# Performance work log

Hardware: AMD Instinct MI355X
Metric: run time of the kernel (lower is better)

## Reference

```python
import jax, jax.numpy as jnp
import numpy as np

B, R, C, D = 4, 64, 64, 512   # batch, rows, cols, hidden_size
H, DH = 4, 128                # num_heads, channels per head
S = R * C                     # flattened attention length (raster order)
NEG = -1e6                    # mask value used by coltran


def setup_inputs():
    key = jax.random.key(0)
    ks = jax.random.split(key, 7)
    def w(k, shape, s=0.02):
        return jax.random.normal(k, shape, jnp.float32) * s
    return dict(
        x=jax.random.normal(ks[0], (B, R, C, D), jnp.float32),
        wq=w(ks[1], (D, H, DH)),
        wk=w(ks[2], (D, H, DH)),
        wv=w(ks[3], (D, H, DH)),
        wo=w(ks[4], (H, DH, D)),
        # relative_attention_bias_i: [num_heads, 2*length] per axis
        # (zero-init in the original; randomized here so the bias path is exercised)
        rel_row=w(ks[5], (H, 2 * R)),
        rel_col=w(ks[6], (H, 2 * C)),
    )


def _axis_bias(w, L):
    """att_utils.relative_attn_bias: [H, 2L] -> [H, Lq, Lk], b[h,q,k] = w[h, L-1 + k - q]."""
    pos = jnp.arange(L)
    idx = (L - 1) + pos[None, :] - pos[:, None]  # [Lq, Lk] in [0, 2L-2]
    return w[:, idx]


def reference(x, wq, wk, wv, wo, rel_row, rel_col):
    # q/k/v projections: contract channel axis into [H, DH]
    q = jnp.einsum('brcd,dhe->brche', x, wq) * (DH ** -0.5)
    k = jnp.einsum('brcd,dhe->brche', x, wk)
    v = jnp.einsum('brcd,dhe->brche', x, wv)
    q = q.reshape(B, S, H, DH)
    k = k.reshape(B, S, H, DH)
    v = v.reshape(B, S, H, DH)

    # factorized N-D relative attention bias -> [H, S, S]
    brow = _axis_bias(rel_row, R)  # [H, R, R]
    bcol = _axis_bias(rel_col, C)  # [H, C, C]
    bias = (brow[:, :, None, :, None] + bcol[:, None, :, None, :]).reshape(H, S, S)

    # 'future' mask in raster order: disallow k > q
    mask = jnp.triu(jnp.full((S, S), NEG, dtype=jnp.float32), 1)

    logits = jnp.einsum('bqhe,bkhe->bhqk', q, k) + bias[None] + mask[None, None]
    p = jax.nn.softmax(logits, axis=-1)
    o = jnp.einsum('bhqk,bkhe->bqhe', p, v)       # weighted sum over keys
    out = jnp.einsum('bqhe,hed->bqd', o, wo)      # final projection, contract_axes=2
    return out.reshape(B, R, C, D)
```

## Files before the change

kernel.cpp:

```cpp
#include <hip/hip_runtime.h>
#include <cstdint>

typedef unsigned short u16;
typedef __attribute__((ext_vector_type(8))) short short8;
typedef __attribute__((ext_vector_type(4))) float f32x4;
typedef __attribute__((ext_vector_type(4))) unsigned short u16x4;
typedef __attribute__((ext_vector_type(2))) float f32x2;
typedef __attribute__((ext_vector_type(2))) __bf16 bf16x2;


__device__ __forceinline__ uint32_t pk2(float a, float b) {
  f32x2 t;
  t[0] = a;
  t[1] = b;
  bf16x2 h = __builtin_convertvector(t, bf16x2);
  return __builtin_bit_cast(uint32_t, h);
}

__device__ __forceinline__ u16 f2b(float f) {
  return __builtin_bit_cast(u16, (__bf16)f);
}

__device__ __forceinline__ uint2 pkbf16x4(f32x4 v, float s) {
  uint2 r;
  r.x = pk2(v[0] * s, v[1] * s);
  r.y = pk2(v[2] * s, v[3] * s);
  return r;
}

#define LDS_FENCE() asm volatile("s_waitcnt lgkmcnt(0)" ::: "memory")

__global__ __launch_bounds__(256) void xcast(const float* __restrict__ x,
                                             u16* __restrict__ xb) {
  const size_t i = (size_t)(blockIdx.x * 256 + threadIdx.x) * 8;
  const float4 a = *(const float4*)(x + i);
  const float4 b = *(const float4*)(x + i + 4);
  uint4 o;
  o.x = pk2(a.x, a.y);
  o.y = pk2(a.z, a.w);
  o.z = pk2(b.x, b.y);
  o.w = pk2(b.z, b.w);
  *(uint4*)(xb + i) = o;
}

__global__ __launch_bounds__(256) void transpose_all(const float* __restrict__ wq,
                                                     const float* __restrict__ wk,
                                                     const float* __restrict__ wv,
                                                     const float* __restrict__ wo,
                                                     u16* __restrict__ wT,
                                                     u16* __restrict__ woT) {
  __shared__ __align__(16) u16 T[64][68];
  const int mtx = blockIdx.y;
  const float* src = (mtx == 0) ? wq : (mtx == 1) ? wk : (mtx == 2) ? wv : wo;
  u16* dst = (mtx < 3) ? (wT + (size_t)mtx * 262144) : woT;
  const int tr = blockIdx.x >> 3, tc = blockIdx.x & 7;
  const int tid = threadIdx.x;
#pragma unroll
  for (int p = 0; p < 4; ++p) {
    int i = p * 256 + tid;
    int row = i >> 4, c4 = i & 15;
    float4 v = *(const float4*)(src + (size_t)(tr * 64 + row) * 512 + tc * 64 + c4 * 4);
    T[c4 * 4 + 0][row] = f2b(v.x);
    T[c4 * 4 + 1][row] = f2b(v.y);
    T[c4 * 4 + 2][row] = f2b(v.z);
    T[c4 * 4 + 3][row] = f2b(v.w);
  }
  __syncthreads();
#pragma unroll
  for (int p = 0; p < 4; ++p) {
    int i = p * 256 + tid;
    int row = i >> 4, c4 = i & 15;
    *(u16x4*)(dst + (size_t)(tc * 64 + row) * 512 + tr * 64 + c4 * 4) =
        *(const u16x4*)&T[row][c4 * 4];
  }
}

__global__ __launch_bounds__(512, 2) void qkv_gemm(const u16* __restrict__ xb,
                                                   const u16* __restrict__ wT_all,
                                                   u16* __restrict__ qbuf,
                                                   u16* __restrict__ kbuf,
                                                   u16* __restrict__ vtbuf) {
  __shared__ __align__(16) u16 smem[128 * 72 + 256 * 72];
  u16* As = smem;
  u16* Bs = smem + 128 * 72;
  const int tid = threadIdx.x;
  const int wave = tid >> 6, lane = tid & 63, quad = lane >> 4, l16 = lane & 15;
  const int wm = wave >> 2, wn = wave & 3;
  const int m0 = blockIdx.x * 128;
  const int which = blockIdx.y >> 1;
  const int n0 = (blockIdx.y & 1) * 256;
  const u16* wTb = wT_all + (size_t)which * 262144 + (size_t)n0 * 512;

  f32x4 acc[4][4];
  const f32x4 fz = {0.f, 0.f, 0.f, 0.f};
#pragma unroll
  for (int i = 0; i < 4; ++i)
#pragma unroll
    for (int j = 0; j < 4; ++j) acc[i][j] = fz;

  for (int k0 = 0; k0 < 512; k0 += 64) {
#pragma unroll
    for (int p = 0; p < 2; ++p) {
      int i = p * 512 + tid, row = i >> 3, c8 = i & 7;
      uint4 v = *(const uint4*)(xb + (size_t)(m0 + row) * 512 + k0 + c8 * 8);
      *(uint4*)&As[row * 72 + c8 * 8] = v;
    }
#pragma unroll
    for (int p = 0; p < 4; ++p) {
      int i = p * 512 + tid, row = i >> 3, c8 = i & 7;
      uint4 v = *(const uint4*)(wTb + (size_t)row * 512 + k0 + c8 * 8);
      *(uint4*)&Bs[row * 72 + c8 * 8] = v;
    }
    __syncthreads();
#pragma unroll
    for (int ks = 0; ks < 2; ++ks) {
      short8 xf[4], wf[4];
#pragma unroll
      for (int mt = 0; mt < 4; ++mt)
        xf[mt] = *(const short8*)&As[(wm * 64 + mt * 16 + l16) * 72 + ks * 32 + quad * 8];
#pragma unroll
      for (int nt = 0; nt < 4; ++nt)
        wf[nt] = *(const short8*)&Bs[(wn * 64 + nt * 16 + l16) * 72 + ks * 32 + quad * 8];
      if (which < 2) {
#pragma unroll
        for (int mt = 0; mt < 4; ++mt)
#pragma unroll
          for (int nt = 0; nt < 4; ++nt)
            acc[mt][nt] = __builtin_amdgcn_mfma_f32_16x16x32_bf16(wf[nt], xf[mt],
                                                                  acc[mt][nt], 0, 0, 0);
      } else {
#pragma unroll
        for (int mt = 0; mt < 4; ++mt)
#pragma unroll
          for (int nt = 0; nt < 4; ++nt)
            acc[mt][nt] = __builtin_amdgcn_mfma_f32_16x16x32_bf16(xf[mt], wf[nt],
                                                                  acc[mt][nt], 0, 0, 0);
      }
    }
    __syncthreads();
  }
  u16* sw = smem + wave * 3072;
  const int dhg0 = n0 + wn * 64;
  const int h = dhg0 >> 7, dhh0 = dhg0 & 127;
  const int bq = m0 >> 12;
  const int bh = bq * 4 + h;
  const int sl0 = (m0 & 4095) + wm * 64;

  if (which < 2) {
    const float scl = (which == 0) ? 0.08838834764831845f : 1.0f;
    u16* dst = (which == 0) ? qbuf : kbuf;
#pragma unroll
    for (int mt = 0; mt < 4; ++mt) {
      LDS_FENCE();
#pragma unroll
      for (int nt = 0; nt < 4; ++nt)
        *(uint2*)&sw[l16 * 68 + nt * 16 + quad * 4] = pkbf16x4(acc[mt][nt], scl);
      LDS_FENCE();
#pragma unroll
      for (int p = 0; p < 2; ++p) {
        const int sr = p * 8 + (lane >> 3), dl = (lane & 7) * 8;
        uint4 v = *(const uint4*)&sw[sr * 68 + dl];
        const int sl = sl0 + mt * 16 + sr;
        *(uint4*)(dst + ((size_t)(bh * 4096 + sl)) * 128 + dhh0 + dl) = v;
      }
    }
  } else {
#pragma unroll
    for (int p2 = 0; p2 < 2; ++p2) {
      LDS_FENCE();
#pragma unroll
      for (int m2 = 0; m2 < 2; ++m2) {
        const int mt = p2 * 2 + m2;
#pragma unroll
        for (int nt = 0; nt < 4; ++nt)
          *(uint2*)&sw[(nt * 16 + l16) * 36 + m2 * 16 + quad * 4] =
              pkbf16x4(acc[mt][nt], 1.0f);
      }
      LDS_FENCE();
#pragma unroll
      for (int j = 0; j < 4; ++j) {
        const int dl = j * 16 + (lane >> 2), so = (lane & 3) * 8;
        uint4 v = *(const uint4*)&sw[dl * 36 + so];
        const int sl = sl0 + p2 * 32 + so;
        *(uint4*)(vtbuf + ((size_t)(bh * 128 + dhh0 + dl)) * 4096 + sl) = v;
      }
    }
  }
}

__global__ __launch_bounds__(512, 4) void attn(const u16* __restrict__ qbuf,
                                               const u16* __restrict__ kbuf,
                                               const u16* __restrict__ vtbuf,
                                               const float* __restrict__ rel_row,
                                               const float* __restrict__ rel_col,
                                               u16* __restrict__ obuf) {
  __shared__ __align__(16) u16 Ks[64][136];
  __shared__ __align__(16) u16 Vt[128][72];
  __shared__ __align__(16) u16 Plds[8][16][72];
  __shared__ float rcol[128];
  __shared__ float rrow[128];

  const int tid = threadIdx.x;
  const int wave = tid >> 6, lane = tid & 63, quad = lane >> 4, l16 = lane & 15;
  const int bh = blockIdx.x & 15;
  const int qt = (blockIdx.x < 256) ? (31 - (blockIdx.x >> 4))
                                    : ((blockIdx.x >> 4) - 16);
  const int b = bh >> 2, h = bh & 3;

  if (tid < 128) rcol[tid] = rel_col[h * 128 + tid];
  else if (tid < 256) rrow[tid - 128] = rel_row[h * 128 + (tid - 128)];

  const int q_loc = wave * 16 + l16;
  const int q_glob = qt * 128 + q_loc;
  const int qr = 2 * qt + (wave >> 2);
  const int qc = q_glob & 63;

  const u16* qrow = qbuf + ((size_t)bh * 4096 + q_glob) * 128;
  short8 qf[4];
#pragma unroll
  for (int ks = 0; ks < 4; ++ks) qf[ks] = *(const short8*)(qrow + ks * 32 + quad * 8);

  __syncthreads();

  const float LOG2E = 1.4426950408889634f;
  float rc2[4][4];
#pragma unroll
  for (int nt = 0; nt < 4; ++nt)
#pragma unroll
    for (int r = 0; r < 4; ++r)
      rc2[nt][r] = rcol[63 + nt * 16 + quad * 4 + r - qc] * LOG2E;

  const f32x4 fz = {0.f, 0.f, 0.f, 0.f};
  f32x4 oacc[8];
#pragma unroll
  for (int i = 0; i < 8; ++i) oacc[i] = fz;
  float l_run = 0.0f;

  const u16* kbase = kbuf + (size_t)bh * 4096 * 128;
  const u16* vbase = vtbuf + (size_t)bh * 128 * 4096;
  const int kr = tid >> 4, kc = (tid & 15) * 8;
  const int vr = tid >> 3, vc = (tid & 7) * 8;

  uint4 kreg0, kreg1, vreg0, vreg1;
  {
    const u16* ksrc = kbase;
    const u16* vsrc = vbase;
    kreg0 = *(const uint4*)(ksrc + kr * 128 + kc);
    kreg1 = *(const uint4*)(ksrc + (32 + kr) * 128 + kc);
    vreg0 = *(const uint4*)(vsrc + (size_t)vr * 4096 + vc);
    vreg1 = *(const uint4*)(vsrc + (size_t)(64 + vr) * 4096 + vc);
  }

  const int ktmax = 2 * qt + 1;
  for (int kt = 0; kt <= ktmax; ++kt) {
    __syncthreads();
    *(uint4*)&Ks[kr][kc] = kreg0;
    *(uint4*)&Ks[32 + kr][kc] = kreg1;
    *(uint4*)&Vt[vr][vc] = vreg0;
    *(uint4*)&Vt[64 + vr][vc] = vreg1;
    __syncthreads();
    if (kt < ktmax) {
      const u16* ksrc = kbase + (kt + 1) * 64 * 128;
      const u16* vsrc = vbase + (kt + 1) * 64;
      kreg0 = *(const uint4*)(ksrc + kr * 128 + kc);
      kreg1 = *(const uint4*)(ksrc + (32 + kr) * 128 + kc);
      vreg0 = *(const uint4*)(vsrc + (size_t)vr * 4096 + vc);
      vreg1 = *(const uint4*)(vsrc + (size_t)(64 + vr) * 4096 + vc);
    }

    if (kt <= qr) {
      f32x4 sacc[4];
#pragma unroll
      for (int nt = 0; nt < 4; ++nt) sacc[nt] = fz;
#pragma unroll
      for (int ks = 0; ks < 4; ++ks)
#pragma unroll
        for (int nt = 0; nt < 4; ++nt) {
          short8 kf = *(const short8*)&Ks[nt * 16 + l16][ks * 32 + quad * 8];
          sacc[nt] = __builtin_amdgcn_mfma_f32_16x16x32_bf16(kf, qf[ks], sacc[nt], 0, 0, 0);
        }

      const float browl = rrow[63 + kt - qr] * LOG2E;
      const bool diag = (kt == qr);
#pragma unroll
      for (int nt = 0; nt < 4; ++nt) {
        f32x4 pv;
#pragma unroll
        for (int r = 0; r < 4; ++r) {
          const int kc2 = nt * 16 + quad * 4 + r;
          float p = __builtin_amdgcn_exp2f(fmaf(sacc[nt][r], LOG2E, rc2[nt][r] + browl));
          if (diag && kc2 > qc) p = 0.0f;
          l_run += p;
          pv[r] = p;
        }
        *(uint2*)&Plds[wave][l16][nt * 16 + quad * 4] = pkbf16x4(pv, 1.0f);
      }

#pragma unroll
      for (int ks2 = 0; ks2 < 2; ++ks2) {
        short8 pf = *(const short8*)&Plds[wave][l16][ks2 * 32 + quad * 8];
#pragma unroll
        for (int mt = 0; mt < 8; ++mt) {
          short8 vf = *(const short8*)&Vt[mt * 16 + l16][ks2 * 32 + quad * 8];
          oacc[mt] = __builtin_amdgcn_mfma_f32_16x16x32_bf16(vf, pf, oacc[mt], 0, 0, 0);
        }
      }
    }
  }

  l_run += __shfl_xor(l_run, 16);
  l_run += __shfl_xor(l_run, 32);
  const float inv_l = 1.0f / l_run;
  u16* orow = obuf + ((size_t)b * 4096 + q_glob) * 512 + h * 128;
#pragma unroll
  for (int mt = 0; mt < 8; ++mt)
    *(uint2*)(orow + mt * 16 + quad * 4) = pkbf16x4(oacc[mt], inv_l);
}

__global__ __launch_bounds__(512, 2) void out_gemm(const u16* __restrict__ obuf,
                                                   const u16* __restrict__ woT,
                                                   float* __restrict__ out) {
  __shared__ __align__(16) u16 smem[128 * 72 + 256 * 72];
  u16* As = smem;
  u16* Bs = smem + 128 * 72;
  const int tid = threadIdx.x;
  const int wave = tid >> 6, lane = tid & 63, quad = lane >> 4, l16 = lane & 15;
  const int wm = wave >> 2, wn = wave & 3;
  const int m0 = blockIdx.x * 128;
  const int n0 = blockIdx.y * 256;

  f32x4 acc[4][4];
  const f32x4 fz = {0.f, 0.f, 0.f, 0.f};
#pragma unroll
  for (int i = 0; i < 4; ++i)
#pragma unroll
    for (int j = 0; j < 4; ++j) acc[i][j] = fz;

  for (int k0 = 0; k0 < 512; k0 += 64) {
#pragma unroll
    for (int p = 0; p < 2; ++p) {
      int i = p * 512 + tid, row = i >> 3, c8 = i & 7;
      uint4 v = *(const uint4*)(obuf + (size_t)(m0 + row) * 512 + k0 + c8 * 8);
      *(uint4*)&As[row * 72 + c8 * 8] = v;
    }
#pragma unroll
    for (int p = 0; p < 4; ++p) {
      int i = p * 512 + tid, row = i >> 3, c8 = i & 7;
      uint4 v = *(const uint4*)(woT + (size_t)(n0 + row) * 512 + k0 + c8 * 8);
      *(uint4*)&Bs[row * 72 + c8 * 8] = v;
    }
    __syncthreads();
#pragma unroll
    for (int ks = 0; ks < 2; ++ks) {
      short8 of[4], wf[4];
#pragma unroll
      for (int mt = 0; mt < 4; ++mt)
        of[mt] = *(const short8*)&As[(wm * 64 + mt * 16 + l16) * 72 + ks * 32 + quad * 8];
#pragma unroll
      for (int nt = 0; nt < 4; ++nt)
        wf[nt] = *(const short8*)&Bs[(wn * 64 + nt * 16 + l16) * 72 + ks * 32 + quad * 8];
#pragma unroll
      for (int mt = 0; mt < 4; ++mt)
#pragma unroll
        for (int nt = 0; nt < 4; ++nt)
          acc[mt][nt] = __builtin_amdgcn_mfma_f32_16x16x32_bf16(wf[nt], of[mt],
                                                                acc[mt][nt], 0, 0, 0);
    }
    __syncthreads();
  }

  float* swf = (float*)smem + wave * 1536;
#pragma unroll
  for (int mt = 0; mt < 4; ++mt) {
    LDS_FENCE();
#pragma unroll
    for (int nt = 0; nt < 4; ++nt)
      *(f32x4*)&swf[l16 * 68 + nt * 16 + quad * 4] = acc[mt][nt];
    LDS_FENCE();
#pragma unroll
    for (int p = 0; p < 4; ++p) {
      const int sr = p * 4 + (lane >> 4), dl = l16 * 4;
      float4 v = *(const float4*)&swf[sr * 68 + dl];
      const int s = m0 + wm * 64 + mt * 16 + sr;
      *(float4*)(out + (size_t)s * 512 + n0 + wn * 64 + dl) = v;
    }
  }
}

extern "C" void kernel_launch(void* const* d_in, const int* in_sizes, int n_in,
                              void* d_out, int out_size, void* d_ws, size_t ws_size,
                              hipStream_t stream) {
  const float* x       = (const float*)d_in[0];
  const float* wq      = (const float*)d_in[1];
  const float* wk      = (const float*)d_in[2];
  const float* wv      = (const float*)d_in[3];
  const float* wo      = (const float*)d_in[4];
  const float* rel_row = (const float*)d_in[5];
  const float* rel_col = (const float*)d_in[6];
  float* out = (float*)d_out;

  char* ws = (char*)d_ws;
  u16* wT    = (u16*)(ws);
  u16* woT   = (u16*)(ws + 1572864);
  u16* qbuf  = (u16*)(ws + 2097152);
  u16* kbuf  = (u16*)(ws + 2097152 + 16777216);
  u16* vtbuf = (u16*)(ws + 2097152 + 2 * 16777216);
  u16* obuf  = (u16*)(ws + 2097152 + 3 * 16777216);
  u16* xb    = obuf;

  xcast<<<4096, 256, 0, stream>>>(x, xb);
  transpose_all<<<dim3(64, 4), 256, 0, stream>>>(wq, wk, wv, wo, wT, woT);
  qkv_gemm<<<dim3(128, 6), 512, 0, stream>>>(xb, wT, qbuf, kbuf, vtbuf);
  attn<<<512, 512, 0, stream>>>(qbuf, kbuf, vtbuf, rel_row, rel_col, obuf);
  out_gemm<<<dim3(128, 2), 512, 0, stream>>>(obuf, woT, out);
}
```

Before: 284.7 us.

## Restructure attention: 64-query blocks, direct global-to-LDS loads, swizzled LDS, register P

The attention kernel now uses 256-thread blocks covering 64 queries each (one image row), launched as 1024 blocks with a four-way load-balanced query-tile ordering. K and V tiles are fetched straight into XOR-swizzled LDS with global_load_lds instead of being staged through registers, and the LOG2E scale is folded into the bias tables. When the 16x16x16 MFMA builtin is available, P stays in registers and feeds the PV MFMA directly, skipping the LDS round trip. Wave priority hints are set around the MFMA loops. In exchange, the next tile is no longer prefetched, so the loads are exposed between the two barriers of each iteration, and K/V tiles are reloaded by twice as many blocks.

```diff
diff --git a/kernel.cpp b/kernel.cpp
--- a/kernel.cpp
+++ b/kernel.cpp
@@ -3,11 +3,18 @@
 
 typedef unsigned short u16;
 typedef __attribute__((ext_vector_type(8))) short short8;
+typedef __attribute__((ext_vector_type(4))) short short4v;
 typedef __attribute__((ext_vector_type(4))) float f32x4;
 typedef __attribute__((ext_vector_type(4))) unsigned short u16x4;
 typedef __attribute__((ext_vector_type(2))) float f32x2;
 typedef __attribute__((ext_vector_type(2))) __bf16 bf16x2;
 
+
+#if defined(__has_builtin)
+#if __has_builtin(__builtin_amdgcn_mfma_f32_16x16x16bf16_1k)
+#define HAVE_MFMA16 1
+#endif
+#endif
 
 __device__ __forceinline__ uint32_t pk2(float a, float b) {
   f32x2 t;
@@ -26,6 +33,12 @@
   r.x = pk2(v[0] * s, v[1] * s);
   r.y = pk2(v[2] * s, v[3] * s);
   return r;
+}
+
+__device__ __forceinline__ void dma16(const u16* g, u16* l) {
+  __builtin_amdgcn_global_load_lds(
+      (const __attribute__((address_space(1))) unsigned int*)(uintptr_t)g,
+      (__attribute__((address_space(3))) unsigned int*)(uintptr_t)l, 16, 0, 0);
 }
 
 #define LDS_FENCE() asm volatile("s_waitcnt lgkmcnt(0)" ::: "memory")
@@ -188,32 +201,34 @@
   }
 }
 
-__global__ __launch_bounds__(512, 4) void attn(const u16* __restrict__ qbuf,
+__global__ __launch_bounds__(256, 4) void attn(const u16* __restrict__ qbuf,
                                                const u16* __restrict__ kbuf,
                                                const u16* __restrict__ vtbuf,
                                                const float* __restrict__ rel_row,
                                                const float* __restrict__ rel_col,
                                                u16* __restrict__ obuf) {
-  __shared__ __align__(16) u16 Ks[64][136];
-  __shared__ __align__(16) u16 Vt[128][72];
-  __shared__ __align__(16) u16 Plds[8][16][72];
+  __shared__ __align__(16) u16 KsF[64 * 128];
+  __shared__ __align__(16) u16 VtF[128 * 64];
+#ifndef HAVE_MFMA16
+  __shared__ __align__(16) u16 Plds[4][16][72];
+#endif
   __shared__ float rcol[128];
   __shared__ float rrow[128];
 
   const int tid = threadIdx.x;
   const int wave = tid >> 6, lane = tid & 63, quad = lane >> 4, l16 = lane & 15;
-  const int bh = blockIdx.x & 15;
-  const int qt = (blockIdx.x < 256) ? (31 - (blockIdx.x >> 4))
-                                    : ((blockIdx.x >> 4) - 16);
+  const int g = blockIdx.x & 255, jq = blockIdx.x >> 8;
+  const int t = g >> 4, bh = g & 15;
+  const int qt = (jq == 0) ? (63 - t) : (jq == 1) ? t : (jq == 2) ? (47 - t) : (16 + t);
   const int b = bh >> 2, h = bh & 3;
 
-  if (tid < 128) rcol[tid] = rel_col[h * 128 + tid];
-  else if (tid < 256) rrow[tid - 128] = rel_row[h * 128 + (tid - 128)];
+  const float LOG2E = 1.4426950408889634f;
+  if (tid < 128) rcol[tid] = rel_col[h * 128 + tid] * LOG2E;
+  else rrow[tid - 128] = rel_row[h * 128 + (tid - 128)] * LOG2E;
 
   const int q_loc = wave * 16 + l16;
-  const int q_glob = qt * 128 + q_loc;
-  const int qr = 2 * qt + (wave >> 2);
-  const int qc = q_glob & 63;
+  const int q_glob = qt * 64 + q_loc;
+  const int qc = q_loc;
 
   const u16* qrow = qbuf + ((size_t)bh * 4096 + q_glob) * 128;
   short8 qf[4];
@@ -222,13 +237,12 @@
 
   __syncthreads();
 
-  const float LOG2E = 1.4426950408889634f;
   float rc2[4][4];
 #pragma unroll
   for (int nt = 0; nt < 4; ++nt)
 #pragma unroll
     for (int r = 0; r < 4; ++r)
-      rc2[nt][r] = rcol[63 + nt * 16 + quad * 4 + r - qc] * LOG2E;
+      rc2[nt][r] = rcol[63 + nt * 16 + quad * 4 + r - qc];
 
   const f32x4 fz = {0.f, 0.f, 0.f, 0.f};
   f32x4 oacc[8];
@@ -238,74 +252,85 @@
 
   const u16* kbase = kbuf + (size_t)bh * 4096 * 128;
   const u16* vbase = vtbuf + (size_t)bh * 128 * 4096;
-  const int kr = tid >> 4, kc = (tid & 15) * 8;
-  const int vr = tid >> 3, vc = (tid & 7) * 8;
-
-  uint4 kreg0, kreg1, vreg0, vreg1;
-  {
-    const u16* ksrc = kbase;
-    const u16* vsrc = vbase;
-    kreg0 = *(const uint4*)(ksrc + kr * 128 + kc);
-    kreg1 = *(const uint4*)(ksrc + (32 + kr) * 128 + kc);
-    vreg0 = *(const uint4*)(vsrc + (size_t)vr * 4096 + vc);
-    vreg1 = *(const uint4*)(vsrc + (size_t)(64 + vr) * 4096 + vc);
-  }
-
-  const int ktmax = 2 * qt + 1;
-  for (int kt = 0; kt <= ktmax; ++kt) {
-    __syncthreads();
-    *(uint4*)&Ks[kr][kc] = kreg0;
-    *(uint4*)&Ks[32 + kr][kc] = kreg1;
-    *(uint4*)&Vt[vr][vc] = vreg0;
-    *(uint4*)&Vt[64 + vr][vc] = vreg1;
-    __syncthreads();
-    if (kt < ktmax) {
-      const u16* ksrc = kbase + (kt + 1) * 64 * 128;
-      const u16* vsrc = vbase + (kt + 1) * 64;
-      kreg0 = *(const uint4*)(ksrc + kr * 128 + kc);
-      kreg1 = *(const uint4*)(ksrc + (32 + kr) * 128 + kc);
-      vreg0 = *(const uint4*)(vsrc + (size_t)vr * 4096 + vc);
-      vreg1 = *(const uint4*)(vsrc + (size_t)(64 + vr) * 4096 + vc);
-    }
-
-    if (kt <= qr) {
-      f32x4 sacc[4];
-#pragma unroll
-      for (int nt = 0; nt < 4; ++nt) sacc[nt] = fz;
-#pragma unroll
-      for (int ks = 0; ks < 4; ++ks)
-#pragma unroll
-        for (int nt = 0; nt < 4; ++nt) {
-          short8 kf = *(const short8*)&Ks[nt * 16 + l16][ks * 32 + quad * 8];
-          sacc[nt] = __builtin_amdgcn_mfma_f32_16x16x32_bf16(kf, qf[ks], sacc[nt], 0, 0, 0);
-        }
-
-      const float browl = rrow[63 + kt - qr] * LOG2E;
-      const bool diag = (kt == qr);
+  const int krow = tid >> 4, kcs = ((tid & 15) ^ (krow & 7)) * 8;
+  const int vrow = tid >> 3, vcs = ((tid & 7) ^ (vrow & 7)) * 8;
+  u16* kdst = KsF + wave * 512;
+  u16* vdst = VtF + wave * 512;
+
+  for (int kt = 0; kt <= qt; ++kt) {
+    __syncthreads();
+    {
+      const u16* ksrc = kbase + (size_t)kt * 8192;
+      const u16* vsrc = vbase + kt * 64;
+#pragma unroll
+      for (int j = 0; j < 4; ++j)
+        dma16(ksrc + (size_t)(j * 16 + krow) * 128 + kcs, kdst + j * 2048);
+#pragma unroll
+      for (int j = 0; j < 4; ++j)
+        dma16(vsrc + (size_t)(j * 32 + vrow) * 4096 + vcs, vdst + j * 2048);
+    }
+    __syncthreads();
+
+    f32x4 sacc[4];
+#pragma unroll
+    for (int nt = 0; nt < 4; ++nt) sacc[nt] = fz;
+    __builtin_amdgcn_s_setprio(1);
+#pragma unroll
+    for (int ks = 0; ks < 4; ++ks)
 #pragma unroll
       for (int nt = 0; nt < 4; ++nt) {
-        f32x4 pv;
-#pragma unroll
-        for (int r = 0; r < 4; ++r) {
-          const int kc2 = nt * 16 + quad * 4 + r;
-          float p = __builtin_amdgcn_exp2f(fmaf(sacc[nt][r], LOG2E, rc2[nt][r] + browl));
-          if (diag && kc2 > qc) p = 0.0f;
-          l_run += p;
-          pv[r] = p;
-        }
-        *(uint2*)&Plds[wave][l16][nt * 16 + quad * 4] = pkbf16x4(pv, 1.0f);
-      }
-
-#pragma unroll
-      for (int ks2 = 0; ks2 < 2; ++ks2) {
-        short8 pf = *(const short8*)&Plds[wave][l16][ks2 * 32 + quad * 8];
-#pragma unroll
-        for (int mt = 0; mt < 8; ++mt) {
-          short8 vf = *(const short8*)&Vt[mt * 16 + l16][ks2 * 32 + quad * 8];
-          oacc[mt] = __builtin_amdgcn_mfma_f32_16x16x32_bf16(vf, pf, oacc[mt], 0, 0, 0);
-        }
-      }
-    }
+        short8 kf = *(const short8*)&KsF[(nt * 16 + l16) * 128 +
+                                         ((ks * 32 + quad * 8) ^ ((l16 & 7) * 8))];
+        sacc[nt] = __builtin_amdgcn_mfma_f32_16x16x32_bf16(kf, qf[ks], sacc[nt], 0, 0, 0);
+      }
+    __builtin_amdgcn_s_setprio(0);
+
+    const float browl = rrow[63 + kt - qt];
+    const bool diag = (kt == qt);
+    uint2 pd[4];
+#pragma unroll
+    for (int nt = 0; nt < 4; ++nt) {
+      f32x4 pv;
+#pragma unroll
+      for (int r = 0; r < 4; ++r) {
+        const int kc2 = nt * 16 + quad * 4 + r;
+        float p = __builtin_amdgcn_exp2f(fmaf(sacc[nt][r], LOG2E, rc2[nt][r] + browl));
+        if (diag && kc2 > qc) p = 0.0f;
+        l_run += p;
+        pv[r] = p;
+      }
+      pd[nt].x = pk2(pv[0], pv[1]);
+      pd[nt].y = pk2(pv[2], pv[3]);
+    }
+
+#ifdef HAVE_MFMA16
+    __builtin_amdgcn_s_setprio(1);
+#pragma unroll
+    for (int nt = 0; nt < 4; ++nt) {
+      short4v pf = __builtin_bit_cast(short4v, pd[nt]);
+#pragma unroll
+      for (int mt = 0; mt < 8; ++mt) {
+        short4v vf = *(const short4v*)&VtF[(mt * 16 + l16) * 64 +
+                                           ((nt * 16 + quad * 4) ^ ((l16 & 7) * 8))];
+        oacc[mt] = __builtin_amdgcn_mfma_f32_16x16x16bf16_1k(vf, pf, oacc[mt], 0, 0, 0);
+      }
+    }
+    __builtin_amdgcn_s_setprio(0);
+#else
+#pragma unroll
+    for (int nt = 0; nt < 4; ++nt)
+      *(uint2*)&Plds[wave][l16][nt * 16 + quad * 4] = pd[nt];
+#pragma unroll
+    for (int ks2 = 0; ks2 < 2; ++ks2) {
+      short8 pf = *(const short8*)&Plds[wave][l16][ks2 * 32 + quad * 8];
+#pragma unroll
+      for (int mt = 0; mt < 8; ++mt) {
+        short8 vf = *(const short8*)&VtF[(mt * 16 + l16) * 64 +
+                                         ((ks2 * 32 + quad * 8) ^ ((l16 & 7) * 8))];
+        oacc[mt] = __builtin_amdgcn_mfma_f32_16x16x32_bf16(vf, pf, oacc[mt], 0, 0, 0);
+      }
+    }
+#endif
   }
 
   l_run += __shfl_xor(l_run, 16);
@@ -411,6 +436,6 @@
   xcast<<<4096, 256, 0, stream>>>(x, xb);
   transpose_all<<<dim3(64, 4), 256, 0, stream>>>(wq, wk, wv, wo, wT, woT);
   qkv_gemm<<<dim3(128, 6), 512, 0, stream>>>(xb, wT, qbuf, kbuf, vtbuf);
-  attn<<<512, 512, 0, stream>>>(qbuf, kbuf, vtbuf, rel_row, rel_col, obuf);
+  attn<<<1024, 256, 0, stream>>>(qbuf, kbuf, vtbuf, rel_row, rel_col, obuf);
   out_gemm<<<dim3(128, 2), 512, 0, stream>>>(obuf, woT, out);
 }
```

Measured after the change: 298.6 us. +4.9%, slower.
